# Optimization experiments

Measured on AMD Instinct MI355X. Metric: run time of the kernel, lower is better.

## Reference

```python
import jax, jax.numpy as jnp
import numpy as np

N = 32768          # nodes
DEG = 16           # fixed in-degree per dst node
E = N * DEG        # edges
IN_FEATS = 256
HEADS = 4
OUT = 64
NUM_CLASSES = 40
SLOPE = 0.2        # leaky_relu negative slope
GM = 0.1           # graph margin
CM = 0.1           # class margin


def setup_inputs() -> dict:
    key = jax.random.key(0)
    ks = jax.random.split(key, 8)
    feat = jax.random.normal(ks[0], (N, IN_FEATS), dtype=jnp.float32)
    label = jax.random.randint(ks[1], (N,), 0, NUM_CLASSES)
    src = jax.random.randint(ks[2], (E,), 0, N)
    # dst sorted with fixed in-degree DEG -> dense mailboxes of shape [N, DEG, ...]
    dst = jnp.repeat(jnp.arange(N), DEG)
    # negative graph: same src, dst permuted (construct_negative_graph, k=1)
    neg_perm = jax.random.permutation(ks[3], E)
    scale_w = (2.0 / (IN_FEATS + HEADS * OUT)) ** 0.5  # xavier-ish
    W = jax.random.normal(ks[4], (HEADS * OUT, IN_FEATS), dtype=jnp.float32) * scale_w
    scale_a = (2.0 / (1 + OUT)) ** 0.5
    attn_l = jax.random.normal(ks[5], (HEADS, OUT), dtype=jnp.float32) * scale_a
    attn_r = jax.random.normal(ks[6], (HEADS, OUT), dtype=jnp.float32) * scale_a
    return {"feat": feat, "label": label, "src": src, "dst": dst,
            "neg_perm": neg_perm, "W": W, "attn_l": attn_l, "attn_r": attn_r}


def _leaky(x):
    return jnp.where(x >= 0, x, SLOPE * x)


def reference(feat, label, src, dst, neg_perm, W, attn_l, attn_r):
    n = feat.shape[0]
    e_count = src.shape[0]
    deg = e_count // n
    H, D = attn_l.shape

    feat_src = (feat @ W.T).reshape(n, H, D)               # [N,H,D]
    el = jnp.einsum('nhd,hd->nh', feat_src, attn_l)        # [N,H]
    er = jnp.einsum('nhd,hd->nh', feat_src, attn_r)        # [N,H]
    e = _leaky(el[src] + er[dst])                          # [E,H]

    # ---- graph loss (negative sampling margin) ----
    neg_dst = dst[neg_perm]
    ne = _leaky(el[src] + er[neg_dst])                     # [E,H]
    pw = e.reshape(n, deg, H)                              # positive msgs per dst
    nw = ne.reshape(n, deg, H)                             # negative msgs per dst
    Lg = jnp.maximum(nw[:, :, None, :] + GM - pw[:, None, :, :], 0.0).sum() / (n * H)

    # ---- boundary (class) loss: same-label vs diff-label neighbors ----
    adj = (label[src] == label[dst]).reshape(n, deg)       # [N,DEG] bool
    # difference[n,a,b,h] = w[n,b,h] + CM - w[n,a,h], valid iff adj[a] & ~adj[b]
    val = jnp.maximum(pw[:, None, :, :] + CM - pw[:, :, None, :], 0.0)
    mask = (adj[:, :, None] & (~adj[:, None, :]))[..., None]
    Lb = jnp.where(mask, val, 0.0).sum() / (n * H)

    # ---- edge softmax over each dst's in-edges + attention-weighted sum ----
    a = jax.nn.softmax(pw, axis=1)                         # [N,DEG,H]
    ft = feat_src[src].reshape(n, deg, H, D)               # gathered src feats
    rst = jnp.einsum('ndh,ndhf->nhf', a, ft)               # [N,H,D]
    return rst, Lg, Lb
```

## Files before the change

kernel.cpp:

```cpp
#include <hip/hip_runtime.h>
#include <hip/hip_bf16.h>

#define N_NODES 32768
#define DEG 16
#define E_EDGES (N_NODES * DEG)
#define HEADS 4
#define OUT_D 64
#define HD 256
#define SLOPE 0.2f
#define GMARG 0.1f
#define CMARG 0.1f
#define LOSS_BLOCKS 2048

typedef float f32x4 __attribute__((ext_vector_type(4)));
typedef int   int4v __attribute__((ext_vector_type(4)));
typedef unsigned short ushort4v __attribute__((ext_vector_type(4)));
typedef unsigned short ushort8v __attribute__((ext_vector_type(8)));
typedef short bf16x8 __attribute__((ext_vector_type(8)));
typedef short short4v __attribute__((ext_vector_type(4)));

__device__ __forceinline__ float bf2f(unsigned short u) {
    return __uint_as_float(((unsigned int)u) << 16);
}
__device__ __forceinline__ unsigned short f2bf(float x) {
    __hip_bfloat16 h = __float2bfloat16(x);
    return __builtin_bit_cast(unsigned short, h);
}
__device__ __forceinline__ short f2bf_s(float x) {
    __hip_bfloat16 h = __float2bfloat16(x);
    return __builtin_bit_cast(short, h);
}
__device__ __forceinline__ float leaky(float x) {
    return x >= 0.f ? x : SLOPE * x;
}
__device__ __forceinline__ void gl_lds16(const void* g, void* l) {
    __builtin_amdgcn_global_load_lds(
        (__attribute__((address_space(1))) void*)(g),
        (__attribute__((address_space(3))) void*)(l), 16, 0, 0);
}

__global__ void badcfg_kernel(float* out, float code) {
    out[0] = code;
}

__global__ __launch_bounds__(256) void convw_kernel(const float* __restrict__ W,
                                                    short* __restrict__ Wb) {
    const int i = (blockIdx.x * 256 + threadIdx.x) * 4;
    f32x4 v = *(const f32x4*)(W + i);
    short4v o;
    o[0] = f2bf_s(v[0]); o[1] = f2bf_s(v[1]); o[2] = f2bf_s(v[2]); o[3] = f2bf_s(v[3]);
    *(short4v*)(Wb + i) = o;
}

__global__ __launch_bounds__(256) void gemm_kernel(const float* __restrict__ feat,
                                                   const short* __restrict__ Wb,
                                                   const float* __restrict__ attn_l,
                                                   const float* __restrict__ attn_r,
                                                   unsigned short* __restrict__ fsb,
                                                   float* __restrict__ el,
                                                   float* __restrict__ er) {
    __shared__ short s_b[2][16384];

    const int tid = threadIdx.x;
    const int wave = tid >> 6;
    const int lane = tid & 63;
    const int row0 = (blockIdx.x * 4 + wave) * 16;
    const int m = lane & 15;
    const int q = lane >> 4;

#pragma unroll
    for (int i = 0; i < 8; ++i) {
        const int sb = wave * 8 + i;
        const int kk2 = sb >> 4, t = sb & 15;
        const short* g = Wb + (size_t)(t * 16 + m) * HD + kk2 * 32 + q * 8;
        gl_lds16(g, &s_b[0][sb * 512]);
    }

    bf16x8 afr[8];
    const float* arow = feat + (size_t)(row0 + m) * HD + q * 8;
#pragma unroll
    for (int kk = 0; kk < 8; ++kk) {
        f32x4 lo = *(const f32x4*)(arow + kk * 32);
        f32x4 hi = *(const f32x4*)(arow + kk * 32 + 4);
        bf16x8 aa;
        aa[0] = f2bf_s(lo[0]); aa[1] = f2bf_s(lo[1]); aa[2] = f2bf_s(lo[2]); aa[3] = f2bf_s(lo[3]);
        aa[4] = f2bf_s(hi[0]); aa[5] = f2bf_s(hi[1]); aa[6] = f2bf_s(hi[2]); aa[7] = f2bf_s(hi[3]);
        afr[kk] = aa;
    }

    f32x4 acc[16];
#pragma unroll
    for (int t = 0; t < 16; ++t) acc[t] = (f32x4)(0.0f);

    __syncthreads();

#pragma unroll
    for (int c = 0; c < 4; ++c) {
        if (c < 3) {
#pragma unroll
            for (int i = 0; i < 8; ++i) {
                const int sb = wave * 8 + i;
                const int kk2 = sb >> 4, t = sb & 15;
                const short* g = Wb + (size_t)(t * 16 + m) * HD + (c + 1) * 64 + kk2 * 32 + q * 8;
                gl_lds16(g, &s_b[(c + 1) & 1][sb * 512]);
            }
        }
        const short* sbc = s_b[c & 1];
#pragma unroll
        for (int kk2 = 0; kk2 < 2; ++kk2) {
            const bf16x8 af = afr[c * 2 + kk2];
#pragma unroll
            for (int t = 0; t < 16; ++t) {
                bf16x8 bfr = *(const bf16x8*)(sbc + ((kk2 * 16 + t) * 64 + lane) * 8);
                acc[t] = __builtin_amdgcn_mfma_f32_16x16x32_bf16(af, bfr, acc[t], 0, 0, 0);
            }
        }
        __syncthreads();
    }

#pragma unroll
    for (int t = 0; t < 16; ++t) {
#pragma unroll
        for (int r = 0; r < 4; ++r) {
            fsb[(size_t)(row0 + q * 4 + r) * HD + t * 16 + m] = f2bf(acc[t][r]);
        }
    }

    float pel[4][4], per_[4][4];
#pragma unroll
    for (int h = 0; h < 4; ++h)
#pragma unroll
        for (int r = 0; r < 4; ++r) { pel[h][r] = 0.f; per_[h][r] = 0.f; }
#pragma unroll
    for (int t = 0; t < 16; ++t) {
        const float al = attn_l[t * 16 + m];
        const float ar = attn_r[t * 16 + m];
        const int h = t >> 2;
#pragma unroll
        for (int r = 0; r < 4; ++r) {
            pel[h][r] += acc[t][r] * al;
            per_[h][r] += acc[t][r] * ar;
        }
    }
#pragma unroll
    for (int mask = 1; mask < 16; mask <<= 1) {
#pragma unroll
        for (int h = 0; h < 4; ++h)
#pragma unroll
            for (int r = 0; r < 4; ++r) {
                pel[h][r] += __shfl_xor(pel[h][r], mask, 64);
                per_[h][r] += __shfl_xor(per_[h][r], mask, 64);
            }
    }
    if (m == 0) {
#pragma unroll
        for (int r = 0; r < 4; ++r) {
            const int node = row0 + q * 4 + r;
            f32x4 vl, vr;
            vl[0] = pel[0][r]; vl[1] = pel[1][r]; vl[2] = pel[2][r]; vl[3] = pel[3][r];
            vr[0] = per_[0][r]; vr[1] = per_[1][r]; vr[2] = per_[2][r]; vr[3] = per_[3][r];
            *(f32x4*)(el + (size_t)node * 4) = vl;
            *(f32x4*)(er + (size_t)node * 4) = vr;
        }
    }
}

__global__ __launch_bounds__(256) void loss_kernel(const int* __restrict__ src,
                                                   const int* __restrict__ perm,
                                                   const int* __restrict__ label,
                                                   const float* __restrict__ el,
                                                   const float* __restrict__ er,
                                                   float* __restrict__ partials) {
    __shared__ float s_pw[16][16][4];
    __shared__ int   s_adj[16][16];
    __shared__ float slg[4], slb[4];

    const int tid = threadIdx.x;
    const int wave = tid >> 6;
    const int lane = tid & 63;
    const int w = lane >> 4;
    const int a = lane & 15;
    const int nl = wave * 4 + w;
    const int n = blockIdx.x * 16 + nl;
    const int e = n * DEG + a;

    const int s  = src[e];
    const int nd = perm[e] >> 4;
    f32x4 els  = *(const f32x4*)(el + (size_t)s * 4);
    f32x4 ern  = *(const f32x4*)(er + (size_t)n * 4);
    f32x4 ernd = *(const f32x4*)(er + (size_t)nd * 4);
    const int adja = (label[s] == label[n]) ? 1 : 0;

    f32x4 pw, nw;
#pragma unroll
    for (int h = 0; h < 4; ++h) {
        pw[h] = leaky(els[h] + ern[h]);
        nw[h] = leaky(els[h] + ernd[h]);
    }
    *(f32x4*)&s_pw[nl][a][0] = pw;
    s_adj[nl][a] = adja;
    __syncthreads();

    float lg = 0.f, lb = 0.f;
#pragma unroll
    for (int b = 0; b < 16; ++b) {
        f32x4 pwb = *(const f32x4*)&s_pw[nl][b][0];
        const int adjb = s_adj[nl][b];
#pragma unroll
        for (int h = 0; h < 4; ++h)
            lg += fmaxf(nw[h] + GMARG - pwb[h], 0.f);
        if (adja && !adjb) {
#pragma unroll
            for (int h = 0; h < 4; ++h)
                lb += fmaxf(pwb[h] + CMARG - pw[h], 0.f);
        }
    }
#pragma unroll
    for (int mask = 1; mask < 64; mask <<= 1) {
        lg += __shfl_xor(lg, mask, 64);
        lb += __shfl_xor(lb, mask, 64);
    }
    if (lane == 0) { slg[wave] = lg; slb[wave] = lb; }
    __syncthreads();
    if (tid == 0) {
        partials[blockIdx.x * 2]     = slg[0] + slg[1] + slg[2] + slg[3];
        partials[blockIdx.x * 2 + 1] = slb[0] + slb[1] + slb[2] + slb[3];
    }
}

__global__ __launch_bounds__(256) void agg_kernel(const int* __restrict__ src,
                                                  const float* __restrict__ el,
                                                  const float* __restrict__ er,
                                                  const unsigned short* __restrict__ fsb,
                                                  float* __restrict__ out) {
    __shared__ float s_a[16][128];
    __shared__ int   s_s[16][128];

    const int tid = threadIdx.x;
    const int cg = blockIdx.x & 7;
    const int ng = blockIdx.x >> 3;
    const int hh = cg >> 1;

    {
        const int nl = tid >> 1;
        const int j0 = (tid & 1) * 8;
        const int n = ng * 128 + nl;
        const int* sp = src + n * DEG + j0;
        int4v sa = *(const int4v*)(sp);
        int4v sb = *(const int4v*)(sp + 4);
        int s8[8];
        s8[0] = sa[0]; s8[1] = sa[1]; s8[2] = sa[2]; s8[3] = sa[3];
        s8[4] = sb[0]; s8[5] = sb[1]; s8[6] = sb[2]; s8[7] = sb[3];
        const float ernh = er[n * 4 + hh];
        float pw[8];
#pragma unroll
        for (int k = 0; k < 8; ++k)
            pw[k] = leaky(el[s8[k] * 4 + hh] + ernh);
        float mx = pw[0];
#pragma unroll
        for (int k = 1; k < 8; ++k) mx = fmaxf(mx, pw[k]);
        mx = fmaxf(mx, __shfl_xor(mx, 1, 64));
        float ee[8], sum = 0.f;
#pragma unroll
        for (int k = 0; k < 8; ++k) { ee[k] = __expf(pw[k] - mx); sum += ee[k]; }
        sum += __shfl_xor(sum, 1, 64);
#pragma unroll
        for (int k = 0; k < 8; ++k) {
            s_a[j0 + k][nl] = ee[k] / sum;
            s_s[j0 + k][nl] = s8[k];
        }
    }
    __syncthreads();

    const int nl2 = tid >> 1;
    const int half = tid & 1;
    const int n2 = ng * 128 + nl2;
    const int chb = cg * 32 + half * 16;

    float acc[16];
#pragma unroll
    for (int k = 0; k < 16; ++k) acc[k] = 0.f;
#pragma unroll 4
    for (int j = 0; j < 16; ++j) {
        const int s2 = s_s[j][nl2];
        const float awj = s_a[j][nl2];
        const unsigned short* rp = fsb + (size_t)s2 * HD + chb;
        ushort8v u0 = *(const ushort8v*)(rp);
        ushort8v u1 = *(const ushort8v*)(rp + 8);
#pragma unroll
        for (int k = 0; k < 8; ++k) acc[k]     += awj * bf2f(u0[k]);
#pragma unroll
        for (int k = 0; k < 8; ++k) acc[8 + k] += awj * bf2f(u1[k]);
    }
    float* op = out + (size_t)n2 * HD + chb;
#pragma unroll
    for (int i = 0; i < 4; ++i) {
        f32x4 v;
        v[0] = acc[i * 4]; v[1] = acc[i * 4 + 1]; v[2] = acc[i * 4 + 2]; v[3] = acc[i * 4 + 3];
        *(f32x4*)(op + i * 4) = v;
    }
}

__global__ __launch_bounds__(256) void finalize_kernel(const float* __restrict__ partials,
                                                       float* __restrict__ out) {
    const int tid = threadIdx.x;
    const int lane = tid & 63;
    const int wave = tid >> 6;
    double lg = 0.0, lb = 0.0;
    for (int i = tid; i < LOSS_BLOCKS; i += 256) {
        lg += (double)partials[i * 2];
        lb += (double)partials[i * 2 + 1];
    }
#pragma unroll
    for (int mask = 1; mask < 64; mask <<= 1) {
        lg += __shfl_xor(lg, mask, 64);
        lb += __shfl_xor(lb, mask, 64);
    }
    __shared__ double slg[4], slb[4];
    if (lane == 0) { slg[wave] = lg; slb[wave] = lb; }
    __syncthreads();
    if (tid == 0) {
        const double scale = 1.0 / (double)((size_t)N_NODES * HEADS);
        out[(size_t)N_NODES * HD]     = (float)((slg[0] + slg[1] + slg[2] + slg[3]) * scale);
        out[(size_t)N_NODES * HD + 1] = (float)((slb[0] + slb[1] + slb[2] + slb[3]) * scale);
    }
}

extern "C" void kernel_launch(void* const* d_in, const int* in_sizes, int n_in,
                              void* d_out, int out_size, void* d_ws, size_t ws_size,
                              hipStream_t stream) {
    const float* feat   = (const float*)d_in[0];
    const int*   label  = (const int*)d_in[1];
    const int*   src    = (const int*)d_in[2];
    const int*   perm   = (const int*)d_in[4];
    const float* W      = (const float*)d_in[5];
    const float* attn_l = (const float*)d_in[6];
    const float* attn_r = (const float*)d_in[7];
    float* out = (float*)d_out;

    const int expect[8] = {8388608, 32768, 524288, 524288, 524288, 65536, 256, 256};
    if (n_in != 8) {
        hipLaunchKernelGGL(badcfg_kernel, dim3(1), dim3(1), 0, stream, out, 60000.f);
        return;
    }
    for (int i = 0; i < 8; ++i) {
        if (in_sizes[i] != expect[i]) {
            hipLaunchKernelGGL(badcfg_kernel, dim3(1), dim3(1), 0, stream, out,
                               65536.f + 256.f * (float)i);
            return;
        }
    }
    if (out_size != N_NODES * HD + 2) {
        hipLaunchKernelGGL(badcfg_kernel, dim3(1), dim3(1), 0, stream, out, 200000.f);
        return;
    }

    char* ws = (char*)d_ws;
    size_t off = 0;
    float* partials = (float*)(ws + off); off += (size_t)LOSS_BLOCKS * 2 * sizeof(float);
    off = (off + 255) & ~(size_t)255;
    short* Wb = (short*)(ws + off); off += (size_t)HD * HD * sizeof(short);
    off = (off + 255) & ~(size_t)255;
    unsigned short* fsb = (unsigned short*)(ws + off); off += (size_t)N_NODES * HD * sizeof(unsigned short);
    float* el = (float*)(ws + off); off += (size_t)N_NODES * HEADS * sizeof(float);
    float* er = (float*)(ws + off); off += (size_t)N_NODES * HEADS * sizeof(float);
    if (off > ws_size) {
        hipLaunchKernelGGL(badcfg_kernel, dim3(1), dim3(1), 0, stream, out, 131072.f);
        return;
    }

    hipLaunchKernelGGL(convw_kernel, dim3(HD * HD / 1024), dim3(256), 0, stream, W, Wb);
    hipLaunchKernelGGL(gemm_kernel, dim3(N_NODES / 64), dim3(256), 0, stream,
                       feat, Wb, attn_l, attn_r, fsb, el, er);
    hipLaunchKernelGGL(loss_kernel, dim3(LOSS_BLOCKS), dim3(256), 0, stream,
                       src, perm, label, el, er, partials);
    hipLaunchKernelGGL(agg_kernel, dim3(2048), dim3(256), 0, stream,
                       src, el, er, fsb, out);
    hipLaunchKernelGGL(finalize_kernel, dim3(1), dim3(256), 0, stream, partials, out);
}
```

Baseline: 180.0 us.

## Compute edge softmax weights in loss kernel and stream them to aggregation

The loss kernel, which already has the positive edge logits, now also computes the per-destination edge-softmax weights with wave shuffles and writes them to a new workspace buffer. The aggregation kernel no longer gathers el/er or recomputes the softmax in a shared-memory prologue, and drops its __syncthreads. It reads src indices and weights directly with nontemporal loads and stores its output nontemporally. In exchange it adds an 8 MB write plus read of attention weights, and each softmax value is fetched once per channel-group block instead of once per node.

```diff
diff --git a/kernel.cpp b/kernel.cpp
--- a/kernel.cpp
+++ b/kernel.cpp
@@ -170,6 +170,7 @@
                                                    const int* __restrict__ label,
                                                    const float* __restrict__ el,
                                                    const float* __restrict__ er,
+                                                   float* __restrict__ aww,
                                                    float* __restrict__ partials) {
     __shared__ float s_pw[16][16][4];
     __shared__ int   s_adj[16][16];
@@ -199,6 +200,26 @@
     }
     *(f32x4*)&s_pw[nl][a][0] = pw;
     s_adj[nl][a] = adja;
+
+    {
+        f32x4 mx = pw;
+#pragma unroll
+        for (int mask = 1; mask < 16; mask <<= 1)
+#pragma unroll
+            for (int h = 0; h < 4; ++h)
+                mx[h] = fmaxf(mx[h], __shfl_xor(mx[h], mask, 64));
+        f32x4 ee, sm;
+#pragma unroll
+        for (int h = 0; h < 4; ++h) { ee[h] = __expf(pw[h] - mx[h]); sm[h] = ee[h]; }
+#pragma unroll
+        for (int mask = 1; mask < 16; mask <<= 1)
+#pragma unroll
+            for (int h = 0; h < 4; ++h)
+                sm[h] += __shfl_xor(sm[h], mask, 64);
+#pragma unroll
+        for (int h = 0; h < 4; ++h)
+            aww[(((size_t)n * 4 + h) << 4) + a] = ee[h] / sm[h];
+    }
     __syncthreads();
 
     float lg = 0.f, lb = 0.f;
@@ -229,75 +250,48 @@
 }
 
 __global__ __launch_bounds__(256) void agg_kernel(const int* __restrict__ src,
-                                                  const float* __restrict__ el,
-                                                  const float* __restrict__ er,
+                                                  const float* __restrict__ aww,
                                                   const unsigned short* __restrict__ fsb,
                                                   float* __restrict__ out) {
-    __shared__ float s_a[16][128];
-    __shared__ int   s_s[16][128];
-
     const int tid = threadIdx.x;
     const int cg = blockIdx.x & 7;
     const int ng = blockIdx.x >> 3;
     const int hh = cg >> 1;
-
-    {
-        const int nl = tid >> 1;
-        const int j0 = (tid & 1) * 8;
-        const int n = ng * 128 + nl;
-        const int* sp = src + n * DEG + j0;
-        int4v sa = *(const int4v*)(sp);
-        int4v sb = *(const int4v*)(sp + 4);
-        int s8[8];
-        s8[0] = sa[0]; s8[1] = sa[1]; s8[2] = sa[2]; s8[3] = sa[3];
-        s8[4] = sb[0]; s8[5] = sb[1]; s8[6] = sb[2]; s8[7] = sb[3];
-        const float ernh = er[n * 4 + hh];
-        float pw[8];
-#pragma unroll
-        for (int k = 0; k < 8; ++k)
-            pw[k] = leaky(el[s8[k] * 4 + hh] + ernh);
-        float mx = pw[0];
-#pragma unroll
-        for (int k = 1; k < 8; ++k) mx = fmaxf(mx, pw[k]);
-        mx = fmaxf(mx, __shfl_xor(mx, 1, 64));
-        float ee[8], sum = 0.f;
-#pragma unroll
-        for (int k = 0; k < 8; ++k) { ee[k] = __expf(pw[k] - mx); sum += ee[k]; }
-        sum += __shfl_xor(sum, 1, 64);
-#pragma unroll
-        for (int k = 0; k < 8; ++k) {
-            s_a[j0 + k][nl] = ee[k] / sum;
-            s_s[j0 + k][nl] = s8[k];
-        }
-    }
-    __syncthreads();
-
     const int nl2 = tid >> 1;
     const int half = tid & 1;
     const int n2 = ng * 128 + nl2;
     const int chb = cg * 32 + half * 16;
 
+    const int* sp = src + n2 * DEG;
+    const float* ap = aww + (((size_t)n2 * 4 + hh) << 4);
+
     float acc[16];
 #pragma unroll
     for (int k = 0; k < 16; ++k) acc[k] = 0.f;
-#pragma unroll 4
-    for (int j = 0; j < 16; ++j) {
-        const int s2 = s_s[j][nl2];
-        const float awj = s_a[j][nl2];
-        const unsigned short* rp = fsb + (size_t)s2 * HD + chb;
-        ushort8v u0 = *(const ushort8v*)(rp);
-        ushort8v u1 = *(const ushort8v*)(rp + 8);
-#pragma unroll
-        for (int k = 0; k < 8; ++k) acc[k]     += awj * bf2f(u0[k]);
-#pragma unroll
-        for (int k = 0; k < 8; ++k) acc[8 + k] += awj * bf2f(u1[k]);
+
+#pragma unroll
+    for (int jo = 0; jo < 4; ++jo) {
+        int4v sv = __builtin_nontemporal_load((const int4v*)(sp + jo * 4));
+        f32x4 av = __builtin_nontemporal_load((const f32x4*)(ap + jo * 4));
+#pragma unroll
+        for (int j2 = 0; j2 < 4; ++j2) {
+            const int s2 = sv[j2];
+            const float awj = av[j2];
+            const unsigned short* rp = fsb + (size_t)s2 * HD + chb;
+            ushort8v u0 = *(const ushort8v*)(rp);
+            ushort8v u1 = *(const ushort8v*)(rp + 8);
+#pragma unroll
+            for (int k = 0; k < 8; ++k) acc[k]     += awj * bf2f(u0[k]);
+#pragma unroll
+            for (int k = 0; k < 8; ++k) acc[8 + k] += awj * bf2f(u1[k]);
+        }
     }
     float* op = out + (size_t)n2 * HD + chb;
 #pragma unroll
     for (int i = 0; i < 4; ++i) {
         f32x4 v;
         v[0] = acc[i * 4]; v[1] = acc[i * 4 + 1]; v[2] = acc[i * 4 + 2]; v[3] = acc[i * 4 + 3];
-        *(f32x4*)(op + i * 4) = v;
+        __builtin_nontemporal_store(v, (f32x4*)(op + i * 4));
     }
 }
 
@@ -364,6 +358,8 @@
     unsigned short* fsb = (unsigned short*)(ws + off); off += (size_t)N_NODES * HD * sizeof(unsigned short);
     float* el = (float*)(ws + off); off += (size_t)N_NODES * HEADS * sizeof(float);
     float* er = (float*)(ws + off); off += (size_t)N_NODES * HEADS * sizeof(float);
+    off = (off + 255) & ~(size_t)255;
+    float* aww = (float*)(ws + off); off += (size_t)N_NODES * HEADS * DEG * sizeof(float);
     if (off > ws_size) {
         hipLaunchKernelGGL(badcfg_kernel, dim3(1), dim3(1), 0, stream, out, 131072.f);
         return;
@@ -373,8 +369,8 @@
     hipLaunchKernelGGL(gemm_kernel, dim3(N_NODES / 64), dim3(256), 0, stream,
                        feat, Wb, attn_l, attn_r, fsb, el, er);
     hipLaunchKernelGGL(loss_kernel, dim3(LOSS_BLOCKS), dim3(256), 0, stream,
-                       src, perm, label, el, er, partials);
+                       src, perm, label, el, er, aww, partials);
     hipLaunchKernelGGL(agg_kernel, dim3(2048), dim3(256), 0, stream,
-                       src, el, er, fsb, out);
+                       src, aww, fsb, out);
     hipLaunchKernelGGL(finalize_kernel, dim3(1), dim3(256), 0, stream, partials, out);
 }
```

New measurement: 210.3 us. 1.17x slower.
